# Kernel tuning notes

Measured on AMD Instinct MI355X. Metric: run time of the kernel, lower is better.

## Reference

```python
import jax, jax.numpy as jnp
import numpy as np

VOCAB = 32000
HID = 512
T_IN = 128
T_OUT = 128
BATCH = 32


def gru_scan(xs, h0, W, U, bi, br):
    """Keras GRUCell (reset_after=True) over time.
    xs: [T, B, H] inputs; h0: [B, H]; W: [H, 3H]; U: [H, 3H]; bi, br: [3H].
    Returns (h_final [B,H], hs [T,B,H])."""
    # input projections for all timesteps at once
    x_proj = jnp.einsum('tbh,hg->tbg', xs, W) + bi  # [T, B, 3H]

    def step(h, xp):
        rec = h @ U + br                      # [B, 3H]
        xz, xr, xh = jnp.split(xp, 3, axis=-1)
        rz, rr, rh = jnp.split(rec, 3, axis=-1)
        z = jax.nn.sigmoid(xz + rz)
        r = jax.nn.sigmoid(xr + rr)
        hh = jnp.tanh(xh + r * rh)
        h_new = z * h + (1.0 - z) * hh
        return h_new, h_new

    h_final, hs = jax.lax.scan(step, h0, x_proj)
    return h_final, hs


def setup_inputs() -> dict:
    key = jax.random.key(0)
    ks = jax.random.split(key, 12)
    s = 0.05
    return {
        'inputs': jax.random.randint(ks[0], (BATCH, T_IN), 0, VOCAB, dtype=jnp.int64 if jax.config.jax_enable_x64 else jnp.int32),
        'emb': jax.random.normal(ks[1], (VOCAB, HID), jnp.float32) * s,
        'enc_W': jax.random.normal(ks[2], (HID, 3 * HID), jnp.float32) * s,
        'enc_U': jax.random.normal(ks[3], (HID, 3 * HID), jnp.float32) * s,
        'enc_bi': jnp.zeros((3 * HID,), jnp.float32),
        'enc_br': jnp.zeros((3 * HID,), jnp.float32),
        'dec_W': jax.random.normal(ks[4], (HID, 3 * HID), jnp.float32) * s,
        'dec_U': jax.random.normal(ks[5], (HID, 3 * HID), jnp.float32) * s,
        'dec_bi': jnp.zeros((3 * HID,), jnp.float32),
        'dec_br': jnp.zeros((3 * HID,), jnp.float32),
        'w_relu': jax.random.normal(ks[6], (HID, HID), jnp.float32) * s,
        'b_relu': jnp.zeros((HID,), jnp.float32),
        'w_out': jax.random.normal(ks[7], (HID, VOCAB), jnp.float32) * s,
        'b_out': jnp.zeros((VOCAB,), jnp.float32),
    }


def reference(inputs, emb, enc_W, enc_U, enc_bi, enc_br,
              dec_W, dec_U, dec_bi, dec_br, w_relu, b_relu, w_out, b_out):
    B = inputs.shape[0]
    # Embedding lookup: [B, T_in, H] -> time-major [T_in, B, H]
    x = jnp.transpose(emb[inputs], (1, 0, 2))
    h0 = jnp.zeros((B, HID), jnp.float32)
    # Encoder GRU -> final state
    h_enc, _ = gru_scan(x, h0, enc_W, enc_U, enc_bi, enc_br)
    # RepeatVector: decoder input is encoder state at every target step
    dec_in = jnp.broadcast_to(h_enc[None], (T_OUT, B, HID))
    # Decoder GRU with fresh zero state, return sequences
    _, hs = gru_scan(dec_in, h0, dec_W, dec_U, dec_bi, dec_br)  # [T_out, B, H]
    hs = jnp.transpose(hs, (1, 0, 2))  # [B, T_out, H]
    # TimeDistributed Dense+relu, then Dense+softmax over vocab
    h1 = jax.nn.relu(jnp.einsum('bth,hk->btk', hs, w_relu) + b_relu)
    logits = jnp.einsum('bth,hv->btv', h1, w_out) + b_out
    return jax.nn.softmax(logits, axis=-1)
```

## Files before the change

kernel.cpp:

```cpp
#include <hip/hip_runtime.h>
#include <stdint.h>

#define VOCAB 32000
#define HID   512
#define G3    1536
#define TT    128
#define BB    32
#define NROW  4096
#define NCB   250

typedef __attribute__((ext_vector_type(8))) short short8;
typedef __attribute__((ext_vector_type(4))) short short4v;
typedef __attribute__((ext_vector_type(4))) float f32x4;
typedef __attribute__((ext_vector_type(2))) unsigned long long u64x2;

__device__ __forceinline__ unsigned short f2bf(float f) {
  unsigned int u = __builtin_bit_cast(unsigned int, f);
  u += 0x7fffu + ((u >> 16) & 1u);
  return (unsigned short)(u >> 16);
}

__device__ __forceinline__ float bf2f(unsigned short s) {
  unsigned int u = ((unsigned int)s) << 16;
  return __builtin_bit_cast(float, u);
}

__device__ __forceinline__ void gload16(const void* g, void* l) {
  __builtin_amdgcn_global_load_lds(
      (const __attribute__((address_space(1))) unsigned int*)g,
      (__attribute__((address_space(3))) unsigned int*)l, 16, 0, 0);
}

__global__ void convert_bf16_k(const float* __restrict__ src,
                               unsigned short* __restrict__ dst, int n) {
  int i = (blockIdx.x * blockDim.x + threadIdx.x) * 8;
  int stride = gridDim.x * blockDim.x * 8;
  for (; i < n; i += stride) {
    float4 a = *(const float4*)(src + i);
    float4 b = *(const float4*)(src + i + 4);
    short8 o;
    o[0] = (short)f2bf(a.x); o[1] = (short)f2bf(a.y);
    o[2] = (short)f2bf(a.z); o[3] = (short)f2bf(a.w);
    o[4] = (short)f2bf(b.x); o[5] = (short)f2bf(b.y);
    o[6] = (short)f2bf(b.z); o[7] = (short)f2bf(b.w);
    *(short8*)(dst + i) = o;
  }
}

__global__ void transpose_bf16_k(const float* __restrict__ src,
                                 unsigned short* __restrict__ dst,
                                 int K, int N) {
  __shared__ float t[64][65];
  int k0 = blockIdx.x * 64, n0 = blockIdx.y * 64;
  int c = threadIdx.x & 15, rr = threadIdx.x >> 4;
#pragma unroll
  for (int i = 0; i < 4; ++i) {
    float4 v = *(const float4*)(src + (size_t)(k0 + rr + 16 * i) * N + n0 + c * 4);
    t[rr + 16 * i][c * 4 + 0] = v.x;
    t[rr + 16 * i][c * 4 + 1] = v.y;
    t[rr + 16 * i][c * 4 + 2] = v.z;
    t[rr + 16 * i][c * 4 + 3] = v.w;
  }
  __syncthreads();
#pragma unroll
  for (int i = 0; i < 4; ++i) {
    short4v o;
#pragma unroll
    for (int j = 0; j < 4; ++j) o[j] = (short)f2bf(t[c * 4 + j][rr + 16 * i]);
    *(short4v*)(dst + (size_t)(n0 + rr + 16 * i) * K + k0 + c * 4) = o;
  }
}

__global__ void embed_k(const int* __restrict__ inputs,
                        const float* __restrict__ emb,
                        unsigned short* __restrict__ xb) {
  int r = blockIdx.x;
  int t = r >> 5, b = r & 31;
  int idx = inputs[b * TT + t];
  const float* src = emb + (size_t)idx * HID;
  unsigned short* dst = xb + (size_t)r * HID;
  int j = threadIdx.x * 4;
  float4 v = *(const float4*)(src + j);
  short4v o;
  o[0] = (short)f2bf(v.x); o[1] = (short)f2bf(v.y);
  o[2] = (short)f2bf(v.z); o[3] = (short)f2bf(v.w);
  *(short4v*)(dst + j) = o;
}

template<int MODE>
__launch_bounds__(256)
__global__ void gemm_bt(const unsigned short* __restrict__ A,
                        const unsigned short* __restrict__ BT,
                        const float* __restrict__ bias,
                        void* __restrict__ Cv,
                        float* __restrict__ partials,
                        int M, int N, int K) {
  __shared__ unsigned short As[8192];
  __shared__ unsigned short Bs[8192];
  __shared__ float rsum[2][128];
  int tid = threadIdx.x;
  int l = tid & 63;
  int w = tid >> 6;
  int wm = w >> 1, wn = w & 1;

  int nwg = (int)(gridDim.x * gridDim.y);
  int id = (int)(blockIdx.y * gridDim.x + blockIdx.x);
  int nid = (id & 7) * (nwg >> 3) + (id >> 3);
  int bx = nid & 31, by = nid >> 5;
  int row0 = bx * 128;
  int col0 = by * 128;

  int sr = (w << 5) + (l >> 3);
  int sg = ((l & 7) ^ ((l >> 3) & 7)) << 3;
  const unsigned short* Ag = A  + (size_t)(row0 + sr) * K + sg;
  const unsigned short* Bg = BT + (size_t)(col0 + sr) * K + sg;

  int cA = l & 15, q = l >> 4, x7 = l & 7;
  const char* asp = (const char*)As;
  const char* bsp = (const char*)Bs;

  f32x4 acc[4][4];
#pragma unroll
  for (int m = 0; m < 4; ++m)
#pragma unroll
    for (int n = 0; n < 4; ++n) acc[m][n] = (f32x4){0.f, 0.f, 0.f, 0.f};

  for (int k0 = 0; k0 < K; k0 += 64) {
    if (k0) __syncthreads();
#pragma unroll
    for (int i = 0; i < 4; ++i) {
      gload16(Ag + (size_t)(i * 8) * K + k0, As + ((w << 2) + i) * 512);
      gload16(Bg + (size_t)(i * 8) * K + k0, Bs + ((w << 2) + i) * 512);
    }
    __syncthreads();
#pragma unroll
    for (int kk = 0; kk < 2; ++kk) {
      int sl = (((kk << 2) + q) ^ x7) << 4;
      short8 af[4], bf[4];
#pragma unroll
      for (int m = 0; m < 4; ++m)
        af[m] = *(const short8*)(asp + (wm * 64 + m * 16 + cA) * 128 + sl);
#pragma unroll
      for (int n = 0; n < 4; ++n)
        bf[n] = *(const short8*)(bsp + (wn * 64 + n * 16 + cA) * 128 + sl);
#pragma unroll
      for (int m = 0; m < 4; ++m)
#pragma unroll
        for (int n = 0; n < 4; ++n)
          acc[m][n] = __builtin_amdgcn_mfma_f32_16x16x32_bf16(af[m], bf[n],
                                                              acc[m][n], 0, 0, 0);
    }
  }

  if (MODE == 0 || MODE == 1) {
#pragma unroll
    for (int m = 0; m < 4; ++m)
#pragma unroll
      for (int n = 0; n < 4; ++n) {
        int col = col0 + wn * 64 + n * 16 + cA;
        float bv = bias[col];
#pragma unroll
        for (int r = 0; r < 4; ++r) {
          int row = row0 + wm * 64 + m * 16 + q * 4 + r;
          float v = acc[m][n][r] + bv;
          if (MODE == 0)
            ((float*)Cv)[(size_t)row * N + col] = v;
          else
            ((unsigned short*)Cv)[(size_t)row * N + col] = f2bf(fmaxf(v, 0.f));
        }
      }
  } else {
    float ps[4][4];
#pragma unroll
    for (int m = 0; m < 4; ++m)
#pragma unroll
      for (int r = 0; r < 4; ++r) ps[m][r] = 0.f;
#pragma unroll
    for (int m = 0; m < 4; ++m)
#pragma unroll
      for (int n = 0; n < 4; ++n) {
        int col = col0 + wn * 64 + n * 16 + cA;
        float bv = bias[col];
#pragma unroll
        for (int r = 0; r < 4; ++r) {
          int row = row0 + wm * 64 + m * 16 + q * 4 + r;
          float lv = acc[m][n][r] + bv;
          float v = __expf(lv);
          if (MODE == 2)
            ((float*)Cv)[(size_t)row * N + col] = v;
          else
            ((unsigned short*)Cv)[(size_t)row * N + col] = f2bf(lv);
          ps[m][r] += v;
        }
      }
#pragma unroll
    for (int mask = 1; mask < 16; mask <<= 1)
#pragma unroll
      for (int m = 0; m < 4; ++m)
#pragma unroll
        for (int r = 0; r < 4; ++r)
          ps[m][r] += __shfl_xor(ps[m][r], mask, 64);
    if (cA == 0) {
#pragma unroll
      for (int m = 0; m < 4; ++m)
#pragma unroll
        for (int r = 0; r < 4; ++r)
          rsum[wn][wm * 64 + m * 16 + q * 4 + r] = ps[m][r];
    }
    __syncthreads();
    if (tid < 128)
      partials[(size_t)by * NROW + row0 + tid] = rsum[0][tid] + rsum[1][tid];
  }
}

__launch_bounds__(256)
__global__ void gemm_small_k(const unsigned short* __restrict__ A,
                             const unsigned short* __restrict__ B,
                             const float* __restrict__ bias,
                             float* __restrict__ C,
                             int M, int N, int K) {
  __shared__ unsigned short As[64][56];
  __shared__ unsigned short Bs[64][56];
  int tid = threadIdx.x;
  int lane = tid & 63;
  int w = tid >> 6;
  int wm = w >> 1, wn = w & 1;
  int row0 = blockIdx.x * 64;
  int n0 = blockIdx.y * 64;

  f32x4 acc[2][2];
#pragma unroll
  for (int a = 0; a < 2; ++a)
#pragma unroll
    for (int c = 0; c < 2; ++c) acc[a][c] = (f32x4){0.f, 0.f, 0.f, 0.f};

  for (int k0 = 0; k0 < K; k0 += 32) {
    {
      int row = tid >> 2;
      int kg = (tid & 3) * 8;
      short8 v = {};
      if (row0 + row < M)
        v = *(const short8*)(A + (size_t)(row0 + row) * K + k0 + kg);
      *(short8*)&As[row][kg] = v;
    }
    {
      int k = tid >> 3;
      int ng = (tid & 7) * 8;
      short8 v = *(const short8*)(B + (size_t)(k0 + k) * N + n0 + ng);
#pragma unroll
      for (int qq = 0; qq < 8; ++qq) Bs[ng + qq][k] = (unsigned short)v[qq];
    }
    __syncthreads();
    int kb = (lane >> 4) * 8;
    short8 af0 = *(const short8*)&As[wm * 32 + (lane & 15)][kb];
    short8 af1 = *(const short8*)&As[wm * 32 + 16 + (lane & 15)][kb];
    short8 bf0 = *(const short8*)&Bs[wn * 32 + (lane & 15)][kb];
    short8 bf1 = *(const short8*)&Bs[wn * 32 + 16 + (lane & 15)][kb];
    acc[0][0] = __builtin_amdgcn_mfma_f32_16x16x32_bf16(af0, bf0, acc[0][0], 0, 0, 0);
    acc[0][1] = __builtin_amdgcn_mfma_f32_16x16x32_bf16(af0, bf1, acc[0][1], 0, 0, 0);
    acc[1][0] = __builtin_amdgcn_mfma_f32_16x16x32_bf16(af1, bf0, acc[1][0], 0, 0, 0);
    acc[1][1] = __builtin_amdgcn_mfma_f32_16x16x32_bf16(af1, bf1, acc[1][1], 0, 0, 0);
    __syncthreads();
  }
#pragma unroll
  for (int tm = 0; tm < 2; ++tm)
#pragma unroll
    for (int tn = 0; tn < 2; ++tn) {
      int col = n0 + wn * 32 + tn * 16 + (lane & 15);
      float bv = bias[col];
#pragma unroll
      for (int r = 0; r < 4; ++r) {
        int row = row0 + wm * 32 + tm * 16 + ((lane >> 4) * 4) + r;
        if (row < M)
          C[(size_t)row * N + col] = acc[tm][tn][r] + bv;
      }
    }
}

template<int XPT, int WRITE_ALL>
__launch_bounds__(512)
__global__ void gru_k(const float* __restrict__ U,
                      const float* __restrict__ xp,
                      const float* __restrict__ br,
                      unsigned short* __restrict__ hpub,
                      unsigned short* __restrict__ hsout,
                      unsigned int* __restrict__ flags) {
  __shared__ unsigned short ub[16 * 3 * 64 * 8];
  __shared__ unsigned short hbuf[16384];
  __shared__ float recbuf[3][32][16];
  int tid = threadIdx.x;
  int lane = tid & 63;
  int w = tid >> 6;
  int g = blockIdx.x;
  char* hbase = (char*)hbuf;

  for (int idx = tid; idx < 16 * 3 * 64 * 8; idx += 512) {
    int i = idx & 7;
    int l = (idx >> 3) & 63;
    int rem = idx >> 9;
    int nt = rem % 3;
    int ks = rem / 3;
    int k = ks * 32 + ((l >> 4) * 8) + i;
    int col = nt * 512 + g * 16 + (l & 15);
    ub[idx] = f2bf(U[(size_t)k * G3 + col]);
  }
  int b = tid >> 4, j = tid & 15;
  float br_z = br[g * 16 + j];
  float br_r = br[512 + g * 16 + j];
  float br_h = br[1024 + g * 16 + j];
  float hreg = 0.f;
  __syncthreads();

  int mt = w / 3, nt = w % 3;
  for (int t = 0; t < TT; ++t) {
    size_t xbase = ((size_t)(t * XPT + b)) * G3 + g * 16 + j;
    float xz = xp[xbase], xr = xp[xbase + 512], xh = xp[xbase + 1024];

    float rz, rr, rh;
    if (t == 0) {
      rz = 0.f; rr = 0.f; rh = 0.f;
    } else {
      {
        const unsigned long long* hr =
            (const unsigned long long*)(hpub + ((t & 1) ? 16384 : 0));
        int r = tid >> 4, s = tid & 15;
        unsigned long long av[8];
#pragma unroll
        for (int k = 0; k < 4; ++k) {
          const unsigned long long* p = hr + (size_t)r * 128 + (s + 16 * k) * 2;
          av[2 * k]     = __hip_atomic_load(p,     __ATOMIC_RELAXED,
                                            __HIP_MEMORY_SCOPE_AGENT);
          av[2 * k + 1] = __hip_atomic_load(p + 1, __ATOMIC_RELAXED,
                                            __HIP_MEMORY_SCOPE_AGENT);
        }
        int rx = (r & 7) << 4;
#pragma unroll
        for (int k = 0; k < 4; ++k) {
          int wb = (r * 1024 + (s + 16 * k) * 16) ^ rx;
          u64x2 v;
          v[0] = av[2 * k];
          v[1] = av[2 * k + 1];
          *(u64x2*)(hbase + wb) = v;
        }
      }
      __syncthreads();

      if (w < 6) {
        int arow = mt * 16 + (lane & 15);
        int rx = (arow & 7) << 4;
        int abase = arow * 1024 + (lane >> 4) * 16;
        f32x4 acc0 = (f32x4){0.f, 0.f, 0.f, 0.f};
        f32x4 acc1 = (f32x4){0.f, 0.f, 0.f, 0.f};
#pragma unroll
        for (int ks = 0; ks < 8; ++ks) {
          short8 af0 = *(const short8*)(hbase + ((abase + ks * 64) ^ rx));
          short8 af1 = *(const short8*)(hbase + ((abase + (ks + 8) * 64) ^ rx));
          short8 bf0 = *(const short8*)&ub[((ks * 3 + nt) * 64 + lane) * 8];
          short8 bf1 = *(const short8*)&ub[(((ks + 8) * 3 + nt) * 64 + lane) * 8];
          acc0 = __builtin_amdgcn_mfma_f32_16x16x32_bf16(af0, bf0, acc0, 0, 0, 0);
          acc1 = __builtin_amdgcn_mfma_f32_16x16x32_bf16(af1, bf1, acc1, 0, 0, 0);
        }
        f32x4 acc = acc0 + acc1;
#pragma unroll
        for (int r = 0; r < 4; ++r)
          recbuf[nt][mt * 16 + (lane >> 4) * 4 + r][lane & 15] = acc[r];
      }
      __syncthreads();
      rz = recbuf[0][b][j];
      rr = recbuf[1][b][j];
      rh = recbuf[2][b][j];
    }

    float z = 1.f / (1.f + __expf(-(xz + rz + br_z)));
    float rg = 1.f / (1.f + __expf(-(xr + rr + br_r)));
    float pre = xh + rg * (rh + br_h);
    pre = fminf(fmaxf(pre, -15.f), 15.f);
    float e2 = __expf(2.f * pre);
    float hh = (e2 - 1.f) / (e2 + 1.f);
    hreg = z * hreg + (1.f - z) * hh;
    unsigned short hb = f2bf(hreg);

    unsigned int hv = (unsigned int)hb;
    unsigned int p1 = (unsigned int)__shfl_xor((int)hv, 1, 64);
    unsigned long long lo = (unsigned long long)((hv & 0xffffu) | (p1 << 16));
    unsigned long long hi = (unsigned long long)__shfl_xor((int)(unsigned int)lo, 2, 64);
    if ((j & 3) == 0) {
      unsigned long long pk = (lo & 0xffffffffull) | (hi << 32);
      unsigned long long* dst = (unsigned long long*)(hpub +
          (((t + 1) & 1) ? 16384 : 0) + b * HID + g * 16 + j);
      __hip_atomic_store(dst, pk, __ATOMIC_RELAXED, __HIP_MEMORY_SCOPE_AGENT);
    }

    if (t + 1 < TT) {
      asm volatile("s_waitcnt vmcnt(0)" ::: "memory");
      __syncthreads();
      if (tid == 0)
        __hip_atomic_store(flags + g * 32, (unsigned)(t + 1),
                           __ATOMIC_RELAXED, __HIP_MEMORY_SCOPE_AGENT);
    }
    if (WRITE_ALL)
      hsout[((size_t)b * TT + t) * HID + g * 16 + j] = hb;
    if (t + 1 < TT) {
      if (lane < 32) {
        const unsigned int* fp = flags + lane * 32;
        while (__hip_atomic_load(fp, __ATOMIC_RELAXED,
                                 __HIP_MEMORY_SCOPE_AGENT) < (unsigned)(t + 1)) {}
      }
    }
  }
}

__global__ void rowsum_k(const float* __restrict__ part, float* __restrict__ inv) {
  int r = blockIdx.x * blockDim.x + threadIdx.x;
  float s = 0.f;
  for (int c = 0; c < NCB; ++c) s += part[(size_t)c * NROW + r];
  inv[r] = 1.f / s;
}

__global__ void norm_k(float* __restrict__ out, const float* __restrict__ inv) {
  const unsigned int total4 = (unsigned int)NROW * (VOCAB / 4);
  unsigned int stride = gridDim.x * blockDim.x;
  for (unsigned int i = blockIdx.x * blockDim.x + threadIdx.x; i < total4;
       i += stride) {
    unsigned int row = i / (VOCAB / 4);
    float s = inv[row];
    float4* p = (float4*)out + i;
    float4 v = *p;
    v.x *= s; v.y *= s; v.z *= s; v.w *= s;
    *p = v;
  }
}

__global__ void norm2_k(const unsigned short* __restrict__ lg,
                        const float* __restrict__ inv,
                        float* __restrict__ out) {
  const unsigned int total8 = (unsigned int)NROW * (VOCAB / 8);
  unsigned int stride = gridDim.x * blockDim.x;
  for (unsigned int i = blockIdx.x * blockDim.x + threadIdx.x; i < total8;
       i += stride) {
    unsigned int row = i / (VOCAB / 8);
    float s = inv[row];
    short8 v = *(const short8*)(lg + (size_t)i * 8);
    float4 a, b;
    a.x = __expf(bf2f((unsigned short)v[0])) * s;
    a.y = __expf(bf2f((unsigned short)v[1])) * s;
    a.z = __expf(bf2f((unsigned short)v[2])) * s;
    a.w = __expf(bf2f((unsigned short)v[3])) * s;
    b.x = __expf(bf2f((unsigned short)v[4])) * s;
    b.y = __expf(bf2f((unsigned short)v[5])) * s;
    b.z = __expf(bf2f((unsigned short)v[6])) * s;
    b.w = __expf(bf2f((unsigned short)v[7])) * s;
    *(float4*)(out + (size_t)i * 8) = a;
    *(float4*)(out + (size_t)i * 8 + 4) = b;
  }
}

extern "C" void kernel_launch(void* const* d_in, const int* in_sizes, int n_in,
                              void* d_out, int out_size, void* d_ws, size_t ws_size,
                              hipStream_t stream) {
  const int*   inputs = (const int*)d_in[0];
  const float* emb    = (const float*)d_in[1];
  const float* encW   = (const float*)d_in[2];
  const float* encU   = (const float*)d_in[3];
  const float* enc_bi = (const float*)d_in[4];
  const float* enc_br = (const float*)d_in[5];
  const float* decW   = (const float*)d_in[6];
  const float* decU   = (const float*)d_in[7];
  const float* dec_bi = (const float*)d_in[8];
  const float* dec_br = (const float*)d_in[9];
  const float* w_relu = (const float*)d_in[10];
  const float* b_relu = (const float*)d_in[11];
  const float* w_out  = (const float*)d_in[12];
  const float* b_out  = (const float*)d_in[13];

  char* ws = (char*)d_ws;
  const size_t o_xproj  = 0;
  const size_t o_xb     = 25165824;
  const size_t o_encWbT = 29360128;
  const size_t o_decWb  = 30932992;
  const size_t o_wrelubT= 32505856;
  const size_t o_woutbT = 33030144;
  const size_t o_decxp  = 65798144;
  const size_t o_hsb    = 65994752;
  const size_t o_h1b    = 70189056;
  const size_t o_part   = 74383360;
  const size_t o_inv    = 82575360;
  const size_t o_hpubE  = 82591744;
  const size_t o_hpubD  = 82657280;
  const size_t o_logit  = 82722816;
  const size_t need_big = o_logit + (size_t)NROW * VOCAB * 2;

  float*          xproj   = (float*)(ws + o_xproj);
  unsigned short* xb      = (unsigned short*)(ws + o_xb);
  unsigned short* encWbT  = (unsigned short*)(ws + o_encWbT);
  unsigned short* decWb   = (unsigned short*)(ws + o_decWb);
  unsigned short* wrelubT = (unsigned short*)(ws + o_wrelubT);
  unsigned short* woutbT  = (unsigned short*)(ws + o_woutbT);
  float*          decxp   = (float*)(ws + o_decxp);
  unsigned short* hsb     = (unsigned short*)(ws + o_hsb);
  unsigned short* h1b     = (unsigned short*)(ws + o_h1b);
  float*          part    = (float*)(ws + o_part);
  float*          inv     = (float*)(ws + o_inv);
  unsigned short* hpubE   = (unsigned short*)(ws + o_hpubE);
  unsigned short* hpubD   = (unsigned short*)(ws + o_hpubD);
  unsigned short* logit   = (unsigned short*)(ws + o_logit);
  unsigned int*   flagsE  = (unsigned int*)(ws + o_part);
  unsigned int*   flagsD  = (unsigned int*)(ws + o_part + 4096);

  (void)hipMemsetAsync(ws + o_part, 0, 8192, stream);
  (void)hipMemsetAsync(ws + o_hpubE, 0, 65536 * 2, stream);

  transpose_bf16_k<<<dim3(8, 24), 256, 0, stream>>>(encW, encWbT, HID, G3);
  transpose_bf16_k<<<dim3(8, 8), 256, 0, stream>>>(w_relu, wrelubT, HID, HID);
  transpose_bf16_k<<<dim3(8, 500), 256, 0, stream>>>(w_out, woutbT, HID, VOCAB);
  convert_bf16_k<<<384, 256, 0, stream>>>(decW, decWb, 512 * G3);

  embed_k<<<4096, 128, 0, stream>>>(inputs, emb, xb);

  gemm_bt<0><<<dim3(32, 12), 256, 0, stream>>>(xb, encWbT, enc_bi, xproj,
                                               nullptr, NROW, G3, HID);
  gru_k<32, 0><<<32, 512, 0, stream>>>(encU, xproj, enc_br, hpubE, nullptr, flagsE);

  gemm_small_k<<<dim3(1, 24), 256, 0, stream>>>(hpubE, decWb, dec_bi, decxp,
                                                BB, G3, HID);
  gru_k<0, 1><<<32, 512, 0, stream>>>(decU, decxp, dec_br, hpubD, hsb, flagsD);

  gemm_bt<1><<<dim3(32, 4), 256, 0, stream>>>(hsb, wrelubT, b_relu, h1b,
                                              nullptr, NROW, HID, HID);

  if (ws_size >= need_big) {
    gemm_bt<3><<<dim3(32, NCB), 256, 0, stream>>>(h1b, woutbT, b_out, logit,
                                                  part, NROW, VOCAB, HID);
    rowsum_k<<<16, 256, 0, stream>>>(part, inv);
    norm2_k<<<2048, 256, 0, stream>>>(logit, inv, (float*)d_out);
  } else {
    gemm_bt<2><<<dim3(32, NCB), 256, 0, stream>>>(h1b, woutbT, b_out, d_out,
                                                  part, NROW, VOCAB, HID);
    rowsum_k<<<16, 256, 0, stream>>>(part, inv);
    norm_k<<<2048, 256, 0, stream>>>((float*)d_out, inv);
  }
}
```

Before: 1.289 ms.

## Overlap weight transposes and conversions with the encoder GRU in one fused launch

The encoder GRU now runs on 32 blocks of a larger 256-block kernel. The other 224 blocks transpose w_out and w_relu to bf16 and convert dec_W, so these preprocessing launches run on otherwise idle CUs during the latency-bound recurrence instead of serially before it. The decoder GRU becomes a non-template kernel that always reads the broadcast decoder input and writes all hidden states. The small-workspace fallback path is removed. This relies on the 32 spinning GRU blocks staying co-resident with the extra blocks, and the conversion work may compete with the recurrence for memory bandwidth.

After: 1.261 ms. 2.2% less time.

```diff
diff --git a/kernel.cpp b/kernel.cpp
--- a/kernel.cpp
+++ b/kernel.cpp
@@ -19,32 +19,26 @@
   u += 0x7fffu + ((u >> 16) & 1u);
   return (unsigned short)(u >> 16);
 }
-
 __device__ __forceinline__ float bf2f(unsigned short s) {
   unsigned int u = ((unsigned int)s) << 16;
   return __builtin_bit_cast(float, u);
 }
-
 __device__ __forceinline__ void gload16(const void* g, void* l) {
   __builtin_amdgcn_global_load_lds(
       (const __attribute__((address_space(1))) unsigned int*)g,
       (__attribute__((address_space(3))) unsigned int*)l, 16, 0, 0);
 }
-
-__global__ void convert_bf16_k(const float* __restrict__ src,
-                               unsigned short* __restrict__ dst, int n) {
-  int i = (blockIdx.x * blockDim.x + threadIdx.x) * 8;
-  int stride = gridDim.x * blockDim.x * 8;
-  for (; i < n; i += stride) {
-    float4 a = *(const float4*)(src + i);
-    float4 b = *(const float4*)(src + i + 4);
-    short8 o;
-    o[0] = (short)f2bf(a.x); o[1] = (short)f2bf(a.y);
-    o[2] = (short)f2bf(a.z); o[3] = (short)f2bf(a.w);
-    o[4] = (short)f2bf(b.x); o[5] = (short)f2bf(b.y);
-    o[6] = (short)f2bf(b.z); o[7] = (short)f2bf(b.w);
-    *(short8*)(dst + i) = o;
-  }
+__device__ __forceinline__ unsigned long long AL64(const unsigned long long* p) {
+  return __hip_atomic_load(p, __ATOMIC_RELAXED, __HIP_MEMORY_SCOPE_AGENT);
+}
+__device__ __forceinline__ unsigned int AL32(const unsigned int* p) {
+  return __hip_atomic_load(p, __ATOMIC_RELAXED, __HIP_MEMORY_SCOPE_AGENT);
+}
+__device__ __forceinline__ void AS64(unsigned long long* p, unsigned long long v) {
+  __hip_atomic_store(p, v, __ATOMIC_RELAXED, __HIP_MEMORY_SCOPE_AGENT);
+}
+__device__ __forceinline__ void AS32(unsigned int* p, unsigned int v) {
+  __hip_atomic_store(p, v, __ATOMIC_RELAXED, __HIP_MEMORY_SCOPE_AGENT);
 }
 
 __global__ void transpose_bf16_k(const float* __restrict__ src,
@@ -227,13 +221,11 @@
   int wm = w >> 1, wn = w & 1;
   int row0 = blockIdx.x * 64;
   int n0 = blockIdx.y * 64;
-
   f32x4 acc[2][2];
 #pragma unroll
   for (int a = 0; a < 2; ++a)
 #pragma unroll
     for (int c = 0; c < 2; ++c) acc[a][c] = (f32x4){0.f, 0.f, 0.f, 0.f};
-
   for (int k0 = 0; k0 < K; k0 += 32) {
     {
       int row = tid >> 2;
@@ -277,7 +269,127 @@
     }
 }
 
-template<int XPT, int WRITE_ALL>
+template<int XPT>
+__device__ void gru_body(char* smem, const float* __restrict__ U,
+                         const float* __restrict__ xp, const float* __restrict__ br,
+                         unsigned short* __restrict__ hpub,
+                         unsigned int* __restrict__ flags) {
+  unsigned short* ub = (unsigned short*)smem;
+  char* hbase = smem + 49152;
+  float (*recbuf)[32][16] = (float (*)[32][16])(smem + 81920);
+  int tid = threadIdx.x;
+  int lane = tid & 63;
+  int w = tid >> 6;
+  int g = blockIdx.x;
+
+  for (int idx = tid; idx < 16 * 3 * 64 * 8; idx += 512) {
+    int i = idx & 7;
+    int l = (idx >> 3) & 63;
+    int rem = idx >> 9;
+    int nt = rem % 3;
+    int ks = rem / 3;
+    int k = ks * 32 + ((l >> 4) * 8) + i;
+    int col = nt * 512 + g * 16 + (l & 15);
+    ub[idx] = f2bf(U[(size_t)k * G3 + col]);
+  }
+  int b = tid >> 4, j = tid & 15;
+  float br_z = br[g * 16 + j];
+  float br_r = br[512 + g * 16 + j];
+  float br_h = br[1024 + g * 16 + j];
+  float hreg = 0.f;
+  __syncthreads();
+
+  int mt = w / 3, nt = w % 3;
+  for (int t = 0; t < TT; ++t) {
+    size_t xbase = ((size_t)(t * XPT + b)) * G3 + g * 16 + j;
+    float xz = xp[xbase], xr = xp[xbase + 512], xh = xp[xbase + 1024];
+
+    float rz, rr, rh;
+    if (t == 0) {
+      rz = 0.f; rr = 0.f; rh = 0.f;
+    } else {
+      {
+        const unsigned long long* hr =
+            (const unsigned long long*)(hpub + ((t & 1) ? 16384 : 0));
+        int r = tid >> 4, s = tid & 15;
+        unsigned long long av[8];
+#pragma unroll
+        for (int k = 0; k < 4; ++k) {
+          const unsigned long long* p = hr + (size_t)r * 128 + (s + 16 * k) * 2;
+          av[2 * k] = AL64(p);
+          av[2 * k + 1] = AL64(p + 1);
+        }
+        int rx = (r & 7) << 4;
+#pragma unroll
+        for (int k = 0; k < 4; ++k) {
+          int wb = (r * 1024 + (s + 16 * k) * 16) ^ rx;
+          u64x2 v;
+          v[0] = av[2 * k];
+          v[1] = av[2 * k + 1];
+          *(u64x2*)(hbase + wb) = v;
+        }
+      }
+      __syncthreads();
+
+      if (w < 6) {
+        int arow = mt * 16 + (lane & 15);
+        int rx = (arow & 7) << 4;
+        int abase = arow * 1024 + (lane >> 4) * 16;
+        f32x4 acc0 = (f32x4){0.f, 0.f, 0.f, 0.f};
+        f32x4 acc1 = (f32x4){0.f, 0.f, 0.f, 0.f};
+#pragma unroll
+        for (int ks = 0; ks < 8; ++ks) {
+          short8 af0 = *(const short8*)(hbase + ((abase + ks * 64) ^ rx));
+          short8 af1 = *(const short8*)(hbase + ((abase + (ks + 8) * 64) ^ rx));
+          short8 bf0 = *(const short8*)&ub[((ks * 3 + nt) * 64 + lane) * 8];
+          short8 bf1 = *(const short8*)&ub[(((ks + 8) * 3 + nt) * 64 + lane) * 8];
+          acc0 = __builtin_amdgcn_mfma_f32_16x16x32_bf16(af0, bf0, acc0, 0, 0, 0);
+          acc1 = __builtin_amdgcn_mfma_f32_16x16x32_bf16(af1, bf1, acc1, 0, 0, 0);
+        }
+        f32x4 acc = acc0 + acc1;
+#pragma unroll
+        for (int r = 0; r < 4; ++r)
+          recbuf[nt][mt * 16 + (lane >> 4) * 4 + r][lane & 15] = acc[r];
+      }
+      __syncthreads();
+      rz = recbuf[0][b][j];
+      rr = recbuf[1][b][j];
+      rh = recbuf[2][b][j];
+    }
+
+    float z = 1.f / (1.f + __expf(-(xz + rz + br_z)));
+    float rg = 1.f / (1.f + __expf(-(xr + rr + br_r)));
+    float pre = xh + rg * (rh + br_h);
+    pre = fminf(fmaxf(pre, -15.f), 15.f);
+    float e2 = __expf(2.f * pre);
+    float hh = (e2 - 1.f) / (e2 + 1.f);
+    hreg = z * hreg + (1.f - z) * hh;
+    unsigned short hb = f2bf(hreg);
+
+    unsigned int hv = (unsigned int)hb;
+    unsigned int p1 = (unsigned int)__shfl_xor((int)hv, 1, 64);
+    unsigned long long lo = (unsigned long long)((hv & 0xffffu) | (p1 << 16));
+    unsigned long long hi =
+        (unsigned long long)(unsigned int)__shfl_xor((int)(unsigned int)lo, 2, 64);
+    if ((j & 3) == 0) {
+      unsigned long long pk = (lo & 0xffffffffull) | (hi << 32);
+      AS64((unsigned long long*)(hpub + (((t + 1) & 1) ? 16384 : 0) +
+                                 b * HID + g * 16 + j), pk);
+    }
+
+    if (t + 1 < TT) {
+      asm volatile("s_waitcnt vmcnt(0)" ::: "memory");
+      __syncthreads();
+      if (tid == 0)
+        AS32(flags + g * 32, (unsigned)(t + 1));
+      if (lane < 32) {
+        const unsigned int* fp = flags + lane * 32;
+        while (AL32(fp) < (unsigned)(t + 1)) {}
+      }
+    }
+  }
+}
+
 __launch_bounds__(512)
 __global__ void gru_k(const float* __restrict__ U,
                       const float* __restrict__ xp,
@@ -313,7 +425,7 @@
 
   int mt = w / 3, nt = w % 3;
   for (int t = 0; t < TT; ++t) {
-    size_t xbase = ((size_t)(t * XPT + b)) * G3 + g * 16 + j;
+    size_t xbase = ((size_t)b) * G3 + g * 16 + j;
     float xz = xp[xbase], xr = xp[xbase + 512], xh = xp[xbase + 1024];
 
     float rz, rr, rh;
@@ -328,10 +440,8 @@
 #pragma unroll
         for (int k = 0; k < 4; ++k) {
           const unsigned long long* p = hr + (size_t)r * 128 + (s + 16 * k) * 2;
-          av[2 * k]     = __hip_atomic_load(p,     __ATOMIC_RELAXED,
-                                            __HIP_MEMORY_SCOPE_AGENT);
-          av[2 * k + 1] = __hip_atomic_load(p + 1, __ATOMIC_RELAXED,
-                                            __HIP_MEMORY_SCOPE_AGENT);
+          av[2 * k] = AL64(p);
+          av[2 * k + 1] = AL64(p + 1);
         }
         int rx = (r & 7) << 4;
 #pragma unroll
@@ -383,29 +493,95 @@
     unsigned int hv = (unsigned int)hb;
     unsigned int p1 = (unsigned int)__shfl_xor((int)hv, 1, 64);
     unsigned long long lo = (unsigned long long)((hv & 0xffffu) | (p1 << 16));
-    unsigned long long hi = (unsigned long long)__shfl_xor((int)(unsigned int)lo, 2, 64);
+    unsigned long long hi =
+        (unsigned long long)(unsigned int)__shfl_xor((int)(unsigned int)lo, 2, 64);
     if ((j & 3) == 0) {
       unsigned long long pk = (lo & 0xffffffffull) | (hi << 32);
-      unsigned long long* dst = (unsigned long long*)(hpub +
-          (((t + 1) & 1) ? 16384 : 0) + b * HID + g * 16 + j);
-      __hip_atomic_store(dst, pk, __ATOMIC_RELAXED, __HIP_MEMORY_SCOPE_AGENT);
+      AS64((unsigned long long*)(hpub + (((t + 1) & 1) ? 16384 : 0) +
+                                 b * HID + g * 16 + j), pk);
     }
 
     if (t + 1 < TT) {
       asm volatile("s_waitcnt vmcnt(0)" ::: "memory");
       __syncthreads();
       if (tid == 0)
-        __hip_atomic_store(flags + g * 32, (unsigned)(t + 1),
-                           __ATOMIC_RELAXED, __HIP_MEMORY_SCOPE_AGENT);
-    }
-    if (WRITE_ALL)
-      hsout[((size_t)b * TT + t) * HID + g * 16 + j] = hb;
+        AS32(flags + g * 32, (unsigned)(t + 1));
+    }
+    hsout[((size_t)b * TT + t) * HID + g * 16 + j] = hb;
     if (t + 1 < TT) {
       if (lane < 32) {
         const unsigned int* fp = flags + lane * 32;
-        while (__hip_atomic_load(fp, __ATOMIC_RELAXED,
-                                 __HIP_MEMORY_SCOPE_AGENT) < (unsigned)(t + 1)) {}
-      }
+        while (AL32(fp) < (unsigned)(t + 1)) {}
+      }
+    }
+  }
+}
+
+__device__ void tr_tile(char* sm, int tid8, const float* __restrict__ src,
+                        unsigned short* __restrict__ dst,
+                        int K, int N, int k0, int n0) {
+  float (*t)[65] = (float (*)[65])sm;
+  int c = tid8 & 15, rr = tid8 >> 4;
+#pragma unroll
+  for (int i = 0; i < 4; ++i) {
+    float4 v = *(const float4*)(src + (size_t)(k0 + rr + 16 * i) * N + n0 + c * 4);
+    t[rr + 16 * i][c * 4 + 0] = v.x;
+    t[rr + 16 * i][c * 4 + 1] = v.y;
+    t[rr + 16 * i][c * 4 + 2] = v.z;
+    t[rr + 16 * i][c * 4 + 3] = v.w;
+  }
+  __syncthreads();
+#pragma unroll
+  for (int i = 0; i < 4; ++i) {
+    short4v o;
+#pragma unroll
+    for (int j = 0; j < 4; ++j) o[j] = (short)f2bf(t[c * 4 + j][rr + 16 * i]);
+    *(short4v*)(dst + (size_t)(n0 + rr + 16 * i) * K + k0 + c * 4) = o;
+  }
+}
+
+__launch_bounds__(512)
+__global__ void enc_fused_k(const float* __restrict__ U,
+                            const float* __restrict__ xp,
+                            const float* __restrict__ br,
+                            unsigned short* __restrict__ hpub,
+                            unsigned int* __restrict__ flags,
+                            const float* __restrict__ w_out,
+                            unsigned short* __restrict__ woutbT,
+                            const float* __restrict__ w_relu,
+                            unsigned short* __restrict__ wrelubT,
+                            const float* __restrict__ decW,
+                            unsigned short* __restrict__ decWb) {
+  __shared__ char smem[88064];
+  if (blockIdx.x < 32) {
+    gru_body<32>(smem, U, xp, br, hpub, flags);
+    return;
+  }
+  int tid = threadIdx.x;
+  int wid = (int)blockIdx.x - 32;
+  int eng = tid >> 8, tid8 = tid & 255;
+  char* sm = smem + eng * 36864;
+  for (int it = 0; it < 10; ++it) {
+    int tk = wid * 2 + eng + it * 448;
+    if (tk < 4000) {
+      tr_tile(sm, tid8, w_out, woutbT, 512, VOCAB, (tk & 7) * 64, (tk >> 3) * 64);
+    } else if (tk < 4064) {
+      int t2 = tk - 4000;
+      tr_tile(sm, tid8, w_relu, wrelubT, 512, 512, (t2 & 7) * 64, (t2 >> 3) * 64);
+    } else if (tk < 4448) {
+      int c = tk - 4064;
+      int base = c * 2048 + tid8 * 8;
+      float4 a = *(const float4*)(decW + base);
+      float4 bq = *(const float4*)(decW + base + 4);
+      short8 o;
+      o[0] = (short)f2bf(a.x); o[1] = (short)f2bf(a.y);
+      o[2] = (short)f2bf(a.z); o[3] = (short)f2bf(a.w);
+      o[4] = (short)f2bf(bq.x); o[5] = (short)f2bf(bq.y);
+      o[6] = (short)f2bf(bq.z); o[7] = (short)f2bf(bq.w);
+      *(short8*)(decWb + base) = o;
+      __syncthreads();
+    } else {
+      __syncthreads();
     }
   }
 }
@@ -417,29 +593,16 @@
   inv[r] = 1.f / s;
 }
 
-__global__ void norm_k(float* __restrict__ out, const float* __restrict__ inv) {
-  const unsigned int total4 = (unsigned int)NROW * (VOCAB / 4);
-  unsigned int stride = gridDim.x * blockDim.x;
-  for (unsigned int i = blockIdx.x * blockDim.x + threadIdx.x; i < total4;
-       i += stride) {
-    unsigned int row = i / (VOCAB / 4);
-    float s = inv[row];
-    float4* p = (float4*)out + i;
-    float4 v = *p;
-    v.x *= s; v.y *= s; v.z *= s; v.w *= s;
-    *p = v;
-  }
-}
-
 __global__ void norm2_k(const unsigned short* __restrict__ lg,
                         const float* __restrict__ inv,
                         float* __restrict__ out) {
-  const unsigned int total8 = (unsigned int)NROW * (VOCAB / 8);
+  const unsigned int C8 = VOCAB / 8;
+  const unsigned int total8 = (unsigned int)NROW * C8;
   unsigned int stride = gridDim.x * blockDim.x;
   for (unsigned int i = blockIdx.x * blockDim.x + threadIdx.x; i < total8;
        i += stride) {
-    unsigned int row = i / (VOCAB / 8);
-    float s = inv[row];
+    unsigned int r = i / C8;
+    float s = inv[r];
     short8 v = *(const short8*)(lg + (size_t)i * 8);
     float4 a, b;
     a.x = __expf(bf2f((unsigned short)v[0])) * s;
@@ -488,7 +651,6 @@
   const size_t o_hpubE  = 82591744;
   const size_t o_hpubD  = 82657280;
   const size_t o_logit  = 82722816;
-  const size_t need_big = o_logit + (size_t)NROW * VOCAB * 2;
 
   float*          xproj   = (float*)(ws + o_xproj);
   unsigned short* xb      = (unsigned short*)(ws + o_xb);
@@ -508,35 +670,27 @@
   unsigned int*   flagsD  = (unsigned int*)(ws + o_part + 4096);
 
   (void)hipMemsetAsync(ws + o_part, 0, 8192, stream);
-  (void)hipMemsetAsync(ws + o_hpubE, 0, 65536 * 2, stream);
+  (void)hipMemsetAsync(ws + o_hpubE, 0, 131072, stream);
 
   transpose_bf16_k<<<dim3(8, 24), 256, 0, stream>>>(encW, encWbT, HID, G3);
-  transpose_bf16_k<<<dim3(8, 8), 256, 0, stream>>>(w_relu, wrelubT, HID, HID);
-  transpose_bf16_k<<<dim3(8, 500), 256, 0, stream>>>(w_out, woutbT, HID, VOCAB);
-  convert_bf16_k<<<384, 256, 0, stream>>>(decW, decWb, 512 * G3);
-
   embed_k<<<4096, 128, 0, stream>>>(inputs, emb, xb);
 
   gemm_bt<0><<<dim3(32, 12), 256, 0, stream>>>(xb, encWbT, enc_bi, xproj,
                                                nullptr, NROW, G3, HID);
-  gru_k<32, 0><<<32, 512, 0, stream>>>(encU, xproj, enc_br, hpubE, nullptr, flagsE);
+
+  enc_fused_k<<<256, 512, 0, stream>>>(encU, xproj, enc_br, hpubE, flagsE,
+                                       w_out, woutbT, w_relu, wrelubT,
+                                       decW, decWb);
 
   gemm_small_k<<<dim3(1, 24), 256, 0, stream>>>(hpubE, decWb, dec_bi, decxp,
                                                 BB, G3, HID);
-  gru_k<0, 1><<<32, 512, 0, stream>>>(decU, decxp, dec_br, hpubD, hsb, flagsD);
+
+  gru_k<<<32, 512, 0, stream>>>(decU, decxp, dec_br, hpubD, hsb, flagsD);
 
   gemm_bt<1><<<dim3(32, 4), 256, 0, stream>>>(hsb, wrelubT, b_relu, h1b,
                                               nullptr, NROW, HID, HID);
-
-  if (ws_size >= need_big) {
-    gemm_bt<3><<<dim3(32, NCB), 256, 0, stream>>>(h1b, woutbT, b_out, logit,
-                                                  part, NROW, VOCAB, HID);
-    rowsum_k<<<16, 256, 0, stream>>>(part, inv);
-    norm2_k<<<2048, 256, 0, stream>>>(logit, inv, (float*)d_out);
-  } else {
-    gemm_bt<2><<<dim3(32, NCB), 256, 0, stream>>>(h1b, woutbT, b_out, d_out,
-                                                  part, NROW, VOCAB, HID);
-    rowsum_k<<<16, 256, 0, stream>>>(part, inv);
-    norm_k<<<2048, 256, 0, stream>>>((float*)d_out, inv);
-  }
-}
+  gemm_bt<3><<<dim3(32, NCB), 256, 0, stream>>>(h1b, woutbT, b_out, logit,
+                                                part, NROW, VOCAB, HID);
+  rowsum_k<<<16, 256, 0, stream>>>(part, inv);
+  norm2_k<<<2048, 256, 0, stream>>>(logit, inv, (float*)d_out);
+}
```
